# Kernel optimization log

Measured on AMD Instinct MI355X. Metric: run time of the kernel, lower is better.

## Reference

```python
import jax, jax.numpy as jnp
import numpy as np

N_NODES = 50000
D_MODEL = 128
N_EDGES = 600000
HIDDEN = 128
EDGE_FEAT = 2 * D_MODEL + 2  # 258


def setup_inputs() -> dict:
    key = jax.random.key(0)
    k = jax.random.split(key, 8)
    H = jax.random.normal(k[0], (N_NODES, D_MODEL), dtype=jnp.float32)
    edge_index = jax.random.randint(k[1], (2, N_EDGES), 0, N_NODES, dtype=jnp.int64)
    S_e = jax.random.uniform(k[2], (N_EDGES,), dtype=jnp.float32)
    F_e = jax.random.uniform(k[3], (N_EDGES,), dtype=jnp.float32)
    W1 = jax.random.normal(k[4], (EDGE_FEAT, HIDDEN), dtype=jnp.float32) * (1.0 / np.sqrt(EDGE_FEAT))
    b1 = jnp.zeros((HIDDEN,), dtype=jnp.float32)
    W2 = jax.random.normal(k[5], (HIDDEN, 1), dtype=jnp.float32) * (1.0 / np.sqrt(HIDDEN))
    b2 = jnp.zeros((1,), dtype=jnp.float32)
    return {"H": H, "edge_index": edge_index, "S_e": S_e, "F_e": F_e,
            "W1": W1, "b1": b1, "W2": W2, "b2": b2}


def reference(H, edge_index, S_e, F_e, W1, b1, W2, b2):
    # Gather endpoint node features: [E, D]
    H_u = H[edge_index[0]]
    H_v = H[edge_index[1]]
    H_diff = jnp.abs(H_u - H_v)
    H_prod = H_u * H_v
    # [E, 2D+2]
    edge_features = jnp.concatenate(
        [H_diff, H_prod, S_e[:, None], F_e[:, None]], axis=1)
    # 2-layer MLP with SiLU (dropout is identity in eval mode)
    h = jax.nn.silu(edge_features @ W1 + b1)
    a_e = (h @ W2 + b2)[:, 0]  # [E]
    return a_e
```

## Files before the change

### kernel.cpp

```cpp
#include <hip/hip_runtime.h>


typedef _Float16       half8   __attribute__((ext_vector_type(8)));
typedef _Float16       half4v  __attribute__((ext_vector_type(4)));
typedef unsigned short ushort8 __attribute__((ext_vector_type(8)));
typedef float          f32x4   __attribute__((ext_vector_type(4)));

#define NSEG    8

__device__ __forceinline__ float silu_f(float x) {
    return x / (1.0f + __expf(-x));
}


__global__ __launch_bounds__(256)
void cvt_zero_kernel(const float* __restrict__ H, _Float16* __restrict__ Hh,
                     int n4, int* __restrict__ zp, int nz) {
    int i = blockIdx.x * blockDim.x + threadIdx.x;
    if (i < nz) zp[i] = 0;
    if (i < n4) {
        const float4 f = ((const float4*)H)[i];
        half4v h;
        h[0] = (_Float16)f.x; h[1] = (_Float16)f.y;
        h[2] = (_Float16)f.z; h[3] = (_Float16)f.w;
        ((half4v*)Hh)[i] = h;
    }
}

__device__ __forceinline__ void canon(int u, int v, int& a, int& b) {
    const int sw = (u ^ v) & 1;
    a = sw ? v : u;
    b = sw ? u : v;
}

__global__ __launch_bounds__(256)
void hist_kernel(const int* __restrict__ eidx, int* __restrict__ hist,
                 int E, int ASZ, int BBINS) {
    int e = blockIdx.x * blockDim.x + threadIdx.x;
    if (e < E) {
        int a, b;
        canon(eidx[e], eidx[E + e], a, b);
        atomicAdd(&hist[(a / ASZ) * BBINS + (b >> 3)], 1);
    }
}

__global__ __launch_bounds__(256)
void scan1_kernel(int* __restrict__ hist, int* __restrict__ bsum, int NB) {
    __shared__ int s[256];
    const int t = threadIdx.x;
    const int i = blockIdx.x * 256 + t;
    const int v = (i < NB) ? hist[i] : 0;
    s[t] = v;
    __syncthreads();
    for (int off = 1; off < 256; off <<= 1) {
        const int x = (t >= off) ? s[t - off] : 0;
        __syncthreads();
        s[t] += x;
        __syncthreads();
    }
    if (i < NB) hist[i] = s[t] - v;
    if (t == 255) bsum[blockIdx.x] = s[255];
}

__global__ __launch_bounds__(256)
void scan2_kernel(int* __restrict__ bsum, int nb1) {
    __shared__ int s[256];
    const int t = threadIdx.x;
    const int v = (t < nb1) ? bsum[t] : 0;
    s[t] = v;
    __syncthreads();
    for (int off = 1; off < 256; off <<= 1) {
        const int x = (t >= off) ? s[t - off] : 0;
        __syncthreads();
        s[t] += x;
        __syncthreads();
    }
    if (t < nb1) bsum[t] = s[t] - v;
}

__global__ __launch_bounds__(256)
void scan3_kernel(int* __restrict__ hist, const int* __restrict__ bsum,
                  int* __restrict__ vbs, int NB, int BBINS, int E) {
    const int i = blockIdx.x * 256 + threadIdx.x;
    if (i < NB) {
        const int val = hist[i] + bsum[blockIdx.x];
        hist[i] = val;
        if (i % BBINS == 0) vbs[i / BBINS] = val;
    }
    if (i == 0) vbs[NSEG] = E;
}

__global__ __launch_bounds__(256)
void scatter_kernel(const int* __restrict__ eidx, const float* __restrict__ Se,
                    const float* __restrict__ Fe, int* __restrict__ ofs,
                    int4* __restrict__ recs, int E, int ASZ, int BBINS) {
    int e = blockIdx.x * blockDim.x + threadIdx.x;
    if (e < E) {
        int a, b;
        canon(eidx[e], eidx[E + e], a, b);
        const int key = (a / ASZ) * BBINS + (b >> 3);
        const int pos = atomicAdd(&ofs[key], 1);
        _Float16 sh = (_Float16)Se[e];
        _Float16 fh = (_Float16)Fe[e];
        unsigned pk = (unsigned)*(unsigned short*)&sh
                    | ((unsigned)*(unsigned short*)&fh << 16);
        recs[pos] = make_int4(a, b, e, (int)pk);
    }
}


template<int NT>
__device__ __forceinline__ void stage_w1(const float* __restrict__ W1,
                                         _Float16* __restrict__ w1t, int tid) {
    const int n = tid & 127;
    const int g = tid >> 7;
    constexpr int GS = NT / 128;
    #pragma unroll
    for (int i = 0; i < 32 / GS; ++i) {
        const int kb = g + i * GS;
        half8 tmp;
        #pragma unroll
        for (int j = 0; j < 8; ++j) {
            const int kp = (kb << 3) + j;
            const int c  = kp >> 5;
            const int r5 = kp & 31;
            const int qq = r5 >> 3;
            const int jj = r5 & 7;
            const int d  = ((c >> 1) << 5) + (qq << 3) + ((c & 1) << 2) + (jj >> 1);
            const int src = ((jj & 1) << 7) + d;
            tmp[j] = (_Float16)W1[src * 128 + n];
        }
        *(half8*)&w1t[n * 256 + ((kb ^ (n & 7)) << 3)] = tmp;
    }
}


__global__ __launch_bounds__(1024, 4)
void edgegate_seg(const _Float16* __restrict__ Hh,
                  const int4*  __restrict__ recs,
                  const int*   __restrict__ vbs,
                  int*         __restrict__ ctr,
                  const float* __restrict__ W1,
                  const float* __restrict__ b1,
                  const float* __restrict__ W2,
                  const float* __restrict__ b2,
                  float*       __restrict__ out)
{
    __shared__ _Float16 w1t[128 * 256];
    __shared__ int tkt[2];
    const int tid = threadIdx.x;
    stage_w1<1024>(W1, w1t, tid);

    int xcd;
    asm volatile("s_getreg_b32 %0, hwreg(HW_REG_XCC_ID)" : "=s"(xcd));
    xcd &= (NSEG - 1);

    __syncthreads();

    const int lane = tid & 63;
    const int wave = tid >> 6;
    const int q    = lane >> 4;
    const int cb   = lane & 15;
    const int swz  = cb & 7;

    int p = 0;
    for (int sidx = 0; sidx < NSEG; ++sidx) {
        const int seg = (xcd + sidx) & (NSEG - 1);
        const int vs  = vbs[seg];
        const int ve  = vbs[seg + 1];
        const int ner = ve - vs;
        if (ner <= 0) continue;
        const int Tt = (ner + 255) >> 8;

        while (true) {
            if (tid == 0) tkt[p] = atomicAdd(&ctr[seg], 1);
            __syncthreads();
            const int t0 = tkt[p];
            p ^= 1;
            if (t0 >= Tt) break;

            const int ebase = vs + (t0 << 8) + (wave << 4);
            const int e = min(ebase + cb, ve - 1);
            const int4 r = recs[e];
            const int a = r.x, b = r.y, oe = r.z;
            const unsigned pk = (unsigned)r.w;
            const unsigned short sl = (unsigned short)(pk & 0xFFFF);
            const unsigned short fl = (unsigned short)(pk >> 16);
            const float Sf = (float)*(const _Float16*)&sl;
            const float Ff = (float)*(const _Float16*)&fl;

            const _Float16* up = Hh + (size_t)a * 128;
            const _Float16* vp = Hh + (size_t)b * 128;

            f32x4 acc[8];
            #pragma unroll
            for (int t = 0; t < 8; ++t) acc[t] = (f32x4){0.f, 0.f, 0.f, 0.f};

            #pragma unroll
            for (int c8 = 0; c8 < 4; ++c8) {
                const half8 u8 = *(const half8*)(up + (c8 << 5) + (q << 3));
                const half8 v8 = *(const half8*)(vp + (c8 << 5) + (q << 3));
                half8 d8 = u8 - v8;
                ushort8 du = *(ushort8*)&d8;
                du = du & (unsigned short)0x7FFF;
                const half8 da = *(half8*)&du;
                const half8 p8 = u8 * v8;

                half8 ae, ao;
                ae[0]=da[0]; ae[1]=p8[0]; ae[2]=da[1]; ae[3]=p8[1];
                ae[4]=da[2]; ae[5]=p8[2]; ae[6]=da[3]; ae[7]=p8[3];
                ao[0]=da[4]; ao[1]=p8[4]; ao[2]=da[5]; ao[3]=p8[5];
                ao[4]=da[6]; ao[5]=p8[6]; ao[6]=da[7]; ao[7]=p8[7];

                const int kb0 = (((c8 << 1) + 0) * 4 + q) ^ swz;
                const int kb1 = (((c8 << 1) + 1) * 4 + q) ^ swz;
                #pragma unroll
                for (int t = 0; t < 8; ++t) {
                    const half8 b0 = *(const half8*)&w1t[((t << 4) + cb) * 256 + (kb0 << 3)];
                    acc[t] = __builtin_amdgcn_mfma_f32_16x16x32_f16(ae, b0, acc[t], 0, 0, 0);
                }
                #pragma unroll
                for (int t = 0; t < 8; ++t) {
                    const half8 b1f = *(const half8*)&w1t[((t << 4) + cb) * 256 + (kb1 << 3)];
                    acc[t] = __builtin_amdgcn_mfma_f32_16x16x32_f16(ao, b1f, acc[t], 0, 0, 0);
                }
            }

            float s_r[4], f_r[4]; int oe_r[4];
            #pragma unroll
            for (int rr = 0; rr < 4; ++rr) {
                const int src = (q << 2) + rr;
                s_r[rr]  = __shfl(Sf, src);
                f_r[rr]  = __shfl(Ff, src);
                oe_r[rr] = __shfl(oe, src);
            }

            float rs[4] = {0.f, 0.f, 0.f, 0.f};
            #pragma unroll
            for (int t = 0; t < 8; ++t) {
                const int col    = (t << 4) + cb;
                const float w256 = W1[32768 + col];
                const float w257 = W1[32896 + col];
                const float b1c  = b1[col];
                const float w2c  = W2[col];
                const f32x4 av = acc[t];
                #pragma unroll
                for (int rr = 0; rr < 4; ++rr)
                    rs[rr] += silu_f(av[rr] + s_r[rr] * w256 + f_r[rr] * w257 + b1c) * w2c;
            }

            #pragma unroll
            for (int off = 1; off < 16; off <<= 1) {
                #pragma unroll
                for (int rr = 0; rr < 4; ++rr) rs[rr] += __shfl_xor(rs[rr], off);
            }

            if (cb == 0) {
                const float b2v = b2[0];
                #pragma unroll
                for (int rr = 0; rr < 4; ++rr) {
                    const int pe = ebase + (q << 2) + rr;
                    if (pe < ve) out[oe_r[rr]] = rs[rr] + b2v;
                }
            }
        }
    }
}


__global__ __launch_bounds__(512, 4)
void edgegate_fb(const float* __restrict__ H,
                 const _Float16* __restrict__ Hh,
                 const int*   __restrict__ eidx,
                 const float* __restrict__ Se,
                 const float* __restrict__ Fe,
                 const float* __restrict__ W1,
                 const float* __restrict__ b1,
                 const float* __restrict__ W2,
                 const float* __restrict__ b2,
                 float*       __restrict__ out,
                 int E, int ntiles, int useF16)
{
    __shared__ _Float16 w1t[128 * 256];
    const int tid = threadIdx.x;
    stage_w1<512>(W1, w1t, tid);
    __syncthreads();

    const int lane = tid & 63;
    const int wave = tid >> 6;
    const int q    = lane >> 4;
    const int cb   = lane & 15;
    const int swz  = cb & 7;

    for (int tile = blockIdx.x; tile < ntiles; tile += gridDim.x) {
        const int ebase = tile * 128 + wave * 16;
        int e = ebase + cb;
        if (e >= E) e = E - 1;
        const int u = eidx[e];
        const int v = eidx[E + e];

        f32x4 acc[8];
        #pragma unroll
        for (int t = 0; t < 8; ++t) acc[t] = (f32x4){0.f, 0.f, 0.f, 0.f};

        #pragma unroll
        for (int c8 = 0; c8 < 4; ++c8) {
            half8 ae, ao;
            if (useF16) {
                const _Float16* up = Hh + (size_t)u * 128;
                const _Float16* vp = Hh + (size_t)v * 128;
                const half8 u8 = *(const half8*)(up + (c8 << 5) + (q << 3));
                const half8 v8 = *(const half8*)(vp + (c8 << 5) + (q << 3));
                half8 d8 = u8 - v8;
                ushort8 du = *(ushort8*)&d8;
                du = du & (unsigned short)0x7FFF;
                const half8 da = *(half8*)&du;
                const half8 p8 = u8 * v8;
                ae[0]=da[0]; ae[1]=p8[0]; ae[2]=da[1]; ae[3]=p8[1];
                ae[4]=da[2]; ae[5]=p8[2]; ae[6]=da[3]; ae[7]=p8[3];
                ao[0]=da[4]; ao[1]=p8[4]; ao[2]=da[5]; ao[3]=p8[5];
                ao[4]=da[6]; ao[5]=p8[6]; ao[6]=da[7]; ao[7]=p8[7];
            } else {
                const float* up = H + (size_t)u * 128;
                const float* vp = H + (size_t)v * 128;
                const float4 uu0 = *(const float4*)(up + (c8 << 5) + (q << 3));
                const float4 vv0 = *(const float4*)(vp + (c8 << 5) + (q << 3));
                const float4 uu1 = *(const float4*)(up + (c8 << 5) + (q << 3) + 4);
                const float4 vv1 = *(const float4*)(vp + (c8 << 5) + (q << 3) + 4);
                ae[0]=(_Float16)fabsf(uu0.x-vv0.x); ae[1]=(_Float16)(uu0.x*vv0.x);
                ae[2]=(_Float16)fabsf(uu0.y-vv0.y); ae[3]=(_Float16)(uu0.y*vv0.y);
                ae[4]=(_Float16)fabsf(uu0.z-vv0.z); ae[5]=(_Float16)(uu0.z*vv0.z);
                ae[6]=(_Float16)fabsf(uu0.w-vv0.w); ae[7]=(_Float16)(uu0.w*vv0.w);
                ao[0]=(_Float16)fabsf(uu1.x-vv1.x); ao[1]=(_Float16)(uu1.x*vv1.x);
                ao[2]=(_Float16)fabsf(uu1.y-vv1.y); ao[3]=(_Float16)(uu1.y*vv1.y);
                ao[4]=(_Float16)fabsf(uu1.z-vv1.z); ao[5]=(_Float16)(uu1.z*vv1.z);
                ao[6]=(_Float16)fabsf(uu1.w-vv1.w); ao[7]=(_Float16)(uu1.w*vv1.w);
            }
            const int kb0 = (((c8 << 1) + 0) * 4 + q) ^ swz;
            const int kb1 = (((c8 << 1) + 1) * 4 + q) ^ swz;
            #pragma unroll
            for (int t = 0; t < 8; ++t) {
                const half8 b0 = *(const half8*)&w1t[((t << 4) + cb) * 256 + (kb0 << 3)];
                acc[t] = __builtin_amdgcn_mfma_f32_16x16x32_f16(ae, b0, acc[t], 0, 0, 0);
            }
            #pragma unroll
            for (int t = 0; t < 8; ++t) {
                const half8 b1f = *(const half8*)&w1t[((t << 4) + cb) * 256 + (kb1 << 3)];
                acc[t] = __builtin_amdgcn_mfma_f32_16x16x32_f16(ao, b1f, acc[t], 0, 0, 0);
            }
        }

        const int e0  = ebase + (q << 2);
        const int e0c = (e0 + 3 < E) ? e0 : (E - 4);
        const float4 s4 = *(const float4*)(Se + e0c);
        const float4 f4 = *(const float4*)(Fe + e0c);

        float rs0 = 0.f, rs1 = 0.f, rs2 = 0.f, rs3 = 0.f;
        #pragma unroll
        for (int t = 0; t < 8; ++t) {
            const int col    = (t << 4) + cb;
            const float w256 = W1[32768 + col];
            const float w257 = W1[32896 + col];
            const float b1c  = b1[col];
            const float w2c  = W2[col];
            const f32x4 av = acc[t];
            rs0 += silu_f(av[0] + s4.x * w256 + f4.x * w257 + b1c) * w2c;
            rs1 += silu_f(av[1] + s4.y * w256 + f4.y * w257 + b1c) * w2c;
            rs2 += silu_f(av[2] + s4.z * w256 + f4.z * w257 + b1c) * w2c;
            rs3 += silu_f(av[3] + s4.w * w256 + f4.w * w257 + b1c) * w2c;
        }
        #pragma unroll
        for (int off = 1; off < 16; off <<= 1) {
            rs0 += __shfl_xor(rs0, off);
            rs1 += __shfl_xor(rs1, off);
            rs2 += __shfl_xor(rs2, off);
            rs3 += __shfl_xor(rs3, off);
        }
        if (cb == 0 && e0 < E) {
            const float b2v = b2[0];
            out[e0]     = rs0 + b2v;
            out[e0 + 1] = rs1 + b2v;
            out[e0 + 2] = rs2 + b2v;
            out[e0 + 3] = rs3 + b2v;
        }
    }
}


static inline size_t align256(size_t x) { return (x + 255) & ~(size_t)255; }

extern "C" void kernel_launch(void* const* d_in, const int* in_sizes, int n_in,
                              void* d_out, int out_size, void* d_ws, size_t ws_size,
                              hipStream_t stream)
{
    const float* H    = (const float*)d_in[0];
    const int*   eidx = (const int*)  d_in[1];
    const float* Se   = (const float*)d_in[2];
    const float* Fe   = (const float*)d_in[3];
    const float* W1   = (const float*)d_in[4];
    const float* b1   = (const float*)d_in[5];
    const float* W2   = (const float*)d_in[6];
    const float* b2   = (const float*)d_in[7];
    float* out = (float*)d_out;

    const int nH     = in_sizes[0];
    const int nNodes = nH / 128;
    const int E      = in_sizes[2];
    const int ntiles = (E + 127) / 128;

    const int ASZ   = (nNodes + NSEG - 1) / NSEG;
    const int BBINS = (nNodes + 7) >> 3;
    const int NB    = NSEG * BBINS;
    const int nb1   = (NB + 255) / 256;

    const size_t hhB    = (size_t)nH * sizeof(_Float16);
    const size_t off_g  = align256(hhB);
    const size_t off_bs = align256(off_g + (size_t)(NB + 8) * 4);
    const size_t off_vb = align256(off_bs + 256 * 4);
    const size_t off_r  = align256(off_vb + 16 * 4);
    const size_t need   = off_r + (size_t)E * sizeof(int4);

    if (ws_size >= need && nb1 <= 256) {
        _Float16* Hh   = (_Float16*)((char*)d_ws);
        int*      hist = (int*)     ((char*)d_ws + off_g);
        int*      ctr  = hist + NB;
        int*      bsum = (int*)     ((char*)d_ws + off_bs);
        int*      vbs  = (int*)     ((char*)d_ws + off_vb);
        int4*     recs = (int4*)    ((char*)d_ws + off_r);

        const int n4 = nH / 4;
        hipLaunchKernelGGL(cvt_zero_kernel, dim3((n4 + 255) / 256), dim3(256), 0,
                           stream, H, Hh, n4, hist, NB + 8);
        hipLaunchKernelGGL(hist_kernel, dim3((E + 255) / 256), dim3(256), 0, stream,
                           eidx, hist, E, ASZ, BBINS);
        hipLaunchKernelGGL(scan1_kernel, dim3(nb1), dim3(256), 0, stream,
                           hist, bsum, NB);
        hipLaunchKernelGGL(scan2_kernel, dim3(1), dim3(256), 0, stream, bsum, nb1);
        hipLaunchKernelGGL(scan3_kernel, dim3(nb1), dim3(256), 0, stream,
                           hist, bsum, vbs, NB, BBINS, E);
        hipLaunchKernelGGL(scatter_kernel, dim3((E + 255) / 256), dim3(256), 0, stream,
                           eidx, Se, Fe, hist, recs, E, ASZ, BBINS);

        hipLaunchKernelGGL(edgegate_seg, dim3(512), dim3(1024), 0, stream,
                           Hh, recs, vbs, ctr, W1, b1, W2, b2, out);
    } else if (ws_size >= hhB) {
        _Float16* Hh = (_Float16*)d_ws;
        const int n4 = nH / 4;
        const int grid = (512 < ntiles) ? 512 : ntiles;
        hipLaunchKernelGGL(cvt_zero_kernel, dim3((n4 + 255) / 256), dim3(256), 0,
                           stream, H, Hh, n4, (int*)nullptr, 0);
        hipLaunchKernelGGL(edgegate_fb, dim3(grid), dim3(512), 0, stream,
                           H, Hh, eidx, Se, Fe, W1, b1, W2, b2, out, E, ntiles, 1);
    } else {
        const int grid = (512 < ntiles) ? 512 : ntiles;
        hipLaunchKernelGGL(edgegate_fb, dim3(grid), dim3(512), 0, stream,
                           H, (const _Float16*)nullptr, eidx, Se, Fe, W1, b1, W2, b2,
                           out, E, ntiles, 0);
    }
}
```

Measured before the change: 303.5 us.

## Process two edge groups per wave and fold scan3 into scan2/scatter

The main edge kernel now runs 512-thread blocks, and each wave handles two 16-edge groups. Every W1 fragment read from LDS is reused across two MFMAs, which halves LDS traffic per edge and gives more independent work to hide gather latency. The separate scan3 pass is removed: scan2 computes the segment bounds directly, and scatter adds the block-level prefix offset on the fly. This saves a kernel launch and a pass over the histogram, at the cost of more accumulator registers per wave and fewer threads per block.

```diff
diff --git a/kernel.cpp b/kernel.cpp
--- a/kernel.cpp
+++ b/kernel.cpp
@@ -63,7 +63,9 @@
 }
 
 __global__ __launch_bounds__(256)
-void scan2_kernel(int* __restrict__ bsum, int nb1) {
+void scan2_kernel(int* __restrict__ bsum, int nb1,
+                  const int* __restrict__ hist, int* __restrict__ vbs,
+                  int BBINS, int E) {
     __shared__ int s[256];
     const int t = threadIdx.x;
     const int v = (t < nb1) ? bsum[t] : 0;
@@ -76,30 +78,26 @@
         __syncthreads();
     }
     if (t < nb1) bsum[t] = s[t] - v;
-}
-
-__global__ __launch_bounds__(256)
-void scan3_kernel(int* __restrict__ hist, const int* __restrict__ bsum,
-                  int* __restrict__ vbs, int NB, int BBINS, int E) {
-    const int i = blockIdx.x * 256 + threadIdx.x;
-    if (i < NB) {
-        const int val = hist[i] + bsum[blockIdx.x];
-        hist[i] = val;
-        if (i % BBINS == 0) vbs[i / BBINS] = val;
-    }
-    if (i == 0) vbs[NSEG] = E;
+    __syncthreads();
+    if (t < NSEG) {
+        const int idx = t * BBINS;
+        vbs[t] = hist[idx] + bsum[idx >> 8];
+    } else if (t == NSEG) {
+        vbs[NSEG] = E;
+    }
 }
 
 __global__ __launch_bounds__(256)
 void scatter_kernel(const int* __restrict__ eidx, const float* __restrict__ Se,
                     const float* __restrict__ Fe, int* __restrict__ ofs,
+                    const int* __restrict__ bsum,
                     int4* __restrict__ recs, int E, int ASZ, int BBINS) {
     int e = blockIdx.x * blockDim.x + threadIdx.x;
     if (e < E) {
         int a, b;
         canon(eidx[e], eidx[E + e], a, b);
         const int key = (a / ASZ) * BBINS + (b >> 3);
-        const int pos = atomicAdd(&ofs[key], 1);
+        const int pos = atomicAdd(&ofs[key], 1) + bsum[key >> 8];
         _Float16 sh = (_Float16)Se[e];
         _Float16 fh = (_Float16)Fe[e];
         unsigned pk = (unsigned)*(unsigned short*)&sh
@@ -109,15 +107,13 @@
 }
 
 
-template<int NT>
 __device__ __forceinline__ void stage_w1(const float* __restrict__ W1,
                                          _Float16* __restrict__ w1t, int tid) {
     const int n = tid & 127;
     const int g = tid >> 7;
-    constexpr int GS = NT / 128;
     #pragma unroll
-    for (int i = 0; i < 32 / GS; ++i) {
-        const int kb = g + i * GS;
+    for (int i = 0; i < 8; ++i) {
+        const int kb = g + (i << 2);
         half8 tmp;
         #pragma unroll
         for (int j = 0; j < 8; ++j) {
@@ -135,7 +131,7 @@
 }
 
 
-__global__ __launch_bounds__(1024, 4)
+__global__ __launch_bounds__(512, 4)
 void edgegate_seg(const _Float16* __restrict__ Hh,
                   const int4*  __restrict__ recs,
                   const int*   __restrict__ vbs,
@@ -149,7 +145,7 @@
     __shared__ _Float16 w1t[128 * 256];
     __shared__ int tkt[2];
     const int tid = threadIdx.x;
-    stage_w1<1024>(W1, w1t, tid);
+    stage_w1(W1, w1t, tid);
 
     int xcd;
     asm volatile("s_getreg_b32 %0, hwreg(HW_REG_XCC_ID)" : "=s"(xcd));
@@ -179,88 +175,103 @@
             p ^= 1;
             if (t0 >= Tt) break;
 
-            const int ebase = vs + (t0 << 8) + (wave << 4);
-            const int e = min(ebase + cb, ve - 1);
-            const int4 r = recs[e];
-            const int a = r.x, b = r.y, oe = r.z;
-            const unsigned pk = (unsigned)r.w;
-            const unsigned short sl = (unsigned short)(pk & 0xFFFF);
-            const unsigned short fl = (unsigned short)(pk >> 16);
-            const float Sf = (float)*(const _Float16*)&sl;
-            const float Ff = (float)*(const _Float16*)&fl;
-
-            const _Float16* up = Hh + (size_t)a * 128;
-            const _Float16* vp = Hh + (size_t)b * 128;
-
-            f32x4 acc[8];
-            #pragma unroll
-            for (int t = 0; t < 8; ++t) acc[t] = (f32x4){0.f, 0.f, 0.f, 0.f};
+            const int ebase = vs + (t0 << 8) + (wave << 5);
+
+            int a_[2], b_[2], oe_[2];
+            float Sf_[2], Ff_[2];
+            const _Float16 *up[2], *vp[2];
+            #pragma unroll
+            for (int g = 0; g < 2; ++g) {
+                const int e = min(ebase + (g << 4) + cb, ve - 1);
+                const int4 r = recs[e];
+                a_[g] = r.x; b_[g] = r.y; oe_[g] = r.z;
+                const unsigned pk = (unsigned)r.w;
+                const unsigned short sl = (unsigned short)(pk & 0xFFFF);
+                const unsigned short fl = (unsigned short)(pk >> 16);
+                Sf_[g] = (float)*(const _Float16*)&sl;
+                Ff_[g] = (float)*(const _Float16*)&fl;
+                up[g] = Hh + (size_t)a_[g] * 128;
+                vp[g] = Hh + (size_t)b_[g] * 128;
+            }
+
+            f32x4 acc[2][8];
+            #pragma unroll
+            for (int g = 0; g < 2; ++g)
+                #pragma unroll
+                for (int t = 0; t < 8; ++t) acc[g][t] = (f32x4){0.f, 0.f, 0.f, 0.f};
 
             #pragma unroll
             for (int c8 = 0; c8 < 4; ++c8) {
-                const half8 u8 = *(const half8*)(up + (c8 << 5) + (q << 3));
-                const half8 v8 = *(const half8*)(vp + (c8 << 5) + (q << 3));
-                half8 d8 = u8 - v8;
-                ushort8 du = *(ushort8*)&d8;
-                du = du & (unsigned short)0x7FFF;
-                const half8 da = *(half8*)&du;
-                const half8 p8 = u8 * v8;
-
-                half8 ae, ao;
-                ae[0]=da[0]; ae[1]=p8[0]; ae[2]=da[1]; ae[3]=p8[1];
-                ae[4]=da[2]; ae[5]=p8[2]; ae[6]=da[3]; ae[7]=p8[3];
-                ao[0]=da[4]; ao[1]=p8[4]; ao[2]=da[5]; ao[3]=p8[5];
-                ao[4]=da[6]; ao[5]=p8[6]; ao[6]=da[7]; ao[7]=p8[7];
+                half8 ae[2], ao[2];
+                #pragma unroll
+                for (int g = 0; g < 2; ++g) {
+                    const half8 u8 = *(const half8*)(up[g] + (c8 << 5) + (q << 3));
+                    const half8 v8 = *(const half8*)(vp[g] + (c8 << 5) + (q << 3));
+                    half8 d8 = u8 - v8;
+                    ushort8 du = *(ushort8*)&d8;
+                    du = du & (unsigned short)0x7FFF;
+                    const half8 da = *(half8*)&du;
+                    const half8 p8 = u8 * v8;
+                    ae[g][0]=da[0]; ae[g][1]=p8[0]; ae[g][2]=da[1]; ae[g][3]=p8[1];
+                    ae[g][4]=da[2]; ae[g][5]=p8[2]; ae[g][6]=da[3]; ae[g][7]=p8[3];
+                    ao[g][0]=da[4]; ao[g][1]=p8[4]; ao[g][2]=da[5]; ao[g][3]=p8[5];
+                    ao[g][4]=da[6]; ao[g][5]=p8[6]; ao[g][6]=da[7]; ao[g][7]=p8[7];
+                }
 
                 const int kb0 = (((c8 << 1) + 0) * 4 + q) ^ swz;
                 const int kb1 = (((c8 << 1) + 1) * 4 + q) ^ swz;
                 #pragma unroll
                 for (int t = 0; t < 8; ++t) {
                     const half8 b0 = *(const half8*)&w1t[((t << 4) + cb) * 256 + (kb0 << 3)];
-                    acc[t] = __builtin_amdgcn_mfma_f32_16x16x32_f16(ae, b0, acc[t], 0, 0, 0);
+                    acc[0][t] = __builtin_amdgcn_mfma_f32_16x16x32_f16(ae[0], b0, acc[0][t], 0, 0, 0);
+                    acc[1][t] = __builtin_amdgcn_mfma_f32_16x16x32_f16(ae[1], b0, acc[1][t], 0, 0, 0);
                 }
                 #pragma unroll
                 for (int t = 0; t < 8; ++t) {
                     const half8 b1f = *(const half8*)&w1t[((t << 4) + cb) * 256 + (kb1 << 3)];
-                    acc[t] = __builtin_amdgcn_mfma_f32_16x16x32_f16(ao, b1f, acc[t], 0, 0, 0);
-                }
-            }
-
-            float s_r[4], f_r[4]; int oe_r[4];
-            #pragma unroll
-            for (int rr = 0; rr < 4; ++rr) {
-                const int src = (q << 2) + rr;
-                s_r[rr]  = __shfl(Sf, src);
-                f_r[rr]  = __shfl(Ff, src);
-                oe_r[rr] = __shfl(oe, src);
-            }
-
-            float rs[4] = {0.f, 0.f, 0.f, 0.f};
-            #pragma unroll
-            for (int t = 0; t < 8; ++t) {
-                const int col    = (t << 4) + cb;
-                const float w256 = W1[32768 + col];
-                const float w257 = W1[32896 + col];
-                const float b1c  = b1[col];
-                const float w2c  = W2[col];
-                const f32x4 av = acc[t];
-                #pragma unroll
-                for (int rr = 0; rr < 4; ++rr)
-                    rs[rr] += silu_f(av[rr] + s_r[rr] * w256 + f_r[rr] * w257 + b1c) * w2c;
-            }
-
-            #pragma unroll
-            for (int off = 1; off < 16; off <<= 1) {
-                #pragma unroll
-                for (int rr = 0; rr < 4; ++rr) rs[rr] += __shfl_xor(rs[rr], off);
-            }
-
-            if (cb == 0) {
-                const float b2v = b2[0];
+                    acc[0][t] = __builtin_amdgcn_mfma_f32_16x16x32_f16(ao[0], b1f, acc[0][t], 0, 0, 0);
+                    acc[1][t] = __builtin_amdgcn_mfma_f32_16x16x32_f16(ao[1], b1f, acc[1][t], 0, 0, 0);
+                }
+            }
+
+            #pragma unroll
+            for (int g = 0; g < 2; ++g) {
+                float s_r[4], f_r[4]; int oe_r[4];
                 #pragma unroll
                 for (int rr = 0; rr < 4; ++rr) {
-                    const int pe = ebase + (q << 2) + rr;
-                    if (pe < ve) out[oe_r[rr]] = rs[rr] + b2v;
+                    const int src = (q << 2) + rr;
+                    s_r[rr]  = __shfl(Sf_[g], src);
+                    f_r[rr]  = __shfl(Ff_[g], src);
+                    oe_r[rr] = __shfl(oe_[g], src);
+                }
+
+                float rs[4] = {0.f, 0.f, 0.f, 0.f};
+                #pragma unroll
+                for (int t = 0; t < 8; ++t) {
+                    const int col    = (t << 4) + cb;
+                    const float w256 = W1[32768 + col];
+                    const float w257 = W1[32896 + col];
+                    const float b1c  = b1[col];
+                    const float w2c  = W2[col];
+                    const f32x4 av = acc[g][t];
+                    #pragma unroll
+                    for (int rr = 0; rr < 4; ++rr)
+                        rs[rr] += silu_f(av[rr] + s_r[rr] * w256 + f_r[rr] * w257 + b1c) * w2c;
+                }
+
+                #pragma unroll
+                for (int off = 1; off < 16; off <<= 1) {
+                    #pragma unroll
+                    for (int rr = 0; rr < 4; ++rr) rs[rr] += __shfl_xor(rs[rr], off);
+                }
+
+                if (cb == 0) {
+                    const float b2v = b2[0];
+                    #pragma unroll
+                    for (int rr = 0; rr < 4; ++rr) {
+                        const int pe = ebase + (g << 4) + (q << 2) + rr;
+                        if (pe < ve) out[oe_r[rr]] = rs[rr] + b2v;
+                    }
                 }
             }
         }
@@ -283,7 +294,7 @@
 {
     __shared__ _Float16 w1t[128 * 256];
     const int tid = threadIdx.x;
-    stage_w1<512>(W1, w1t, tid);
+    stage_w1(W1, w1t, tid);
     __syncthreads();
 
     const int lane = tid & 63;
@@ -435,13 +446,12 @@
                            eidx, hist, E, ASZ, BBINS);
         hipLaunchKernelGGL(scan1_kernel, dim3(nb1), dim3(256), 0, stream,
                            hist, bsum, NB);
-        hipLaunchKernelGGL(scan2_kernel, dim3(1), dim3(256), 0, stream, bsum, nb1);
-        hipLaunchKernelGGL(scan3_kernel, dim3(nb1), dim3(256), 0, stream,
-                           hist, bsum, vbs, NB, BBINS, E);
+        hipLaunchKernelGGL(scan2_kernel, dim3(1), dim3(256), 0, stream,
+                           bsum, nb1, hist, vbs, BBINS, E);
         hipLaunchKernelGGL(scatter_kernel, dim3((E + 255) / 256), dim3(256), 0, stream,
-                           eidx, Se, Fe, hist, recs, E, ASZ, BBINS);
-
-        hipLaunchKernelGGL(edgegate_seg, dim3(512), dim3(1024), 0, stream,
+                           eidx, Se, Fe, hist, bsum, recs, E, ASZ, BBINS);
+
+        hipLaunchKernelGGL(edgegate_seg, dim3(512), dim3(512), 0, stream,
                            Hh, recs, vbs, ctr, W1, b1, W2, b2, out);
     } else if (ws_size >= hhB) {
         _Float16* Hh = (_Float16*)d_ws;
```

Result: no change. 307.4 us (+1.3%).
